# Optimization experiments

Measured on AMD Instinct MI355X. Metric: run time of the kernel, lower is better.

## Reference

```python
import jax, jax.numpy as jnp
import numpy as np

B, T, D, H = 2, 2048, 1024, 16
DH = D // H  # 64


def setup_inputs() -> dict:
    key = jax.random.key(0)
    ks = jax.random.split(key, 11)
    s = 1.0 / np.sqrt(D)
    return {
        "q": jax.random.normal(ks[0], (B, T, D), jnp.float32),
        "k": jax.random.normal(ks[1], (B, T, D), jnp.float32),
        "v": jax.random.normal(ks[2], (B, T, D), jnp.float32),
        "Wq": jax.random.normal(ks[3], (D, D), jnp.float32) * s,
        "bq": jnp.zeros((D,), jnp.float32),
        "Wk": jax.random.normal(ks[4], (D, D), jnp.float32) * s,
        "bk": jnp.zeros((D,), jnp.float32),
        "Wv": jax.random.normal(ks[5], (D, D), jnp.float32) * s,
        "bv": jnp.zeros((D,), jnp.float32),
        "Wo": jax.random.normal(ks[6], (D, D), jnp.float32) * s,
        "bo": jnp.zeros((D,), jnp.float32),
    }


def reference(q, k, v, Wq, bq, Wk, bk, Wv, bv, Wo, bo):
    Bq, Tq, _ = q.shape
    Tk = k.shape[1]
    # projections, split heads: [B, H, T, DH]
    qh = (q @ Wq + bq).reshape(Bq, Tq, H, DH).transpose(0, 2, 1, 3)
    kh = (k @ Wk + bk).reshape(Bq, Tk, H, DH).transpose(0, 2, 1, 3)
    vh = (v @ Wv + bv).reshape(Bq, Tk, H, DH).transpose(0, 2, 1, 3)
    # scores [B, H, Tq, Tk]
    scores = jnp.einsum("bhqd,bhkd->bhqk", qh, kh) / np.sqrt(DH)
    # causal mask with diagonal offset Tk - Tq (matches torch.tril semantics)
    ii = jnp.arange(Tq)[:, None]
    jj = jnp.arange(Tk)[None, :]
    causal = jj <= ii + (Tk - Tq)
    scores = jnp.where(causal, scores, -jnp.inf)
    attn = jax.nn.softmax(scores, axis=-1)
    x = jnp.einsum("bhqk,bhkd->bhqd", attn, vh)  # [B, H, Tq, DH]
    x = x.transpose(0, 2, 1, 3).reshape(Bq, Tq, H * DH)
    return x @ Wo + bo
```

## Files before the change

### kernel.cpp

```cpp
#include <hip/hip_runtime.h>

typedef unsigned short u16;
typedef unsigned int   u32;
typedef __attribute__((ext_vector_type(8)))  short short8;
typedef __attribute__((ext_vector_type(4)))  float f32x4;
typedef __attribute__((ext_vector_type(16))) float f32x16;
typedef __attribute__((ext_vector_type(2)))  u32 uint2v;
typedef __attribute__((ext_vector_type(4)))  u32 uint4v;

#define DEV __device__ __forceinline__

DEV u16 f2bf(float f) {
    u32 u = __builtin_bit_cast(u32, f);
    return (u16)((u + 0x7fffu + ((u >> 16) & 1u)) >> 16);
}
DEV float bf2f(u32 u) { return __builtin_bit_cast(float, u << 16); }
DEV u32 cvtpk(float a, float b) {
    u32 r;
    asm("v_cvt_pk_bf16_f32 %0, %1, %2" : "=v"(r) : "v"(a), "v"(b));
    return r;
}
typedef const __attribute__((address_space(1))) u32 g_u32;
typedef __attribute__((address_space(3))) u32 l_u32;
DEV void gload16(const u16* g, u16* l) {
    __builtin_amdgcn_global_load_lds((g_u32*)g, (l_u32*)l, 16, 0, 0);
}


DEV void gemm_body(const u16* __restrict__ Apk, const u16* __restrict__ Bpk,
                   const float* __restrict__ bias, float oscale, void* C_,
                   int omode) {
    const int m0 = blockIdx.y * 128, n0 = blockIdx.x * 128;
    const int t = threadIdx.x, lane = t & 63, w = t >> 6;
    const int wm = w >> 1, wn = w & 1;
    const int l15 = lane & 15, l4 = lane >> 4;
    __shared__ __align__(16) u16 As[128 * 32];
    __shared__ __align__(16) u16 Bs[128 * 32];
    f32x4 acc[4][4] = {};

    const int rtA = m0 >> 4, rtB = n0 >> 4;
    for (int k0 = 0; k0 < 1024; k0 += 32) {
        const int ct = k0 >> 5;
        #pragma unroll
        for (int rnd = 0; rnd < 2; rnd++) {
            int cc = rnd * 256 + t, s = cc >> 6, l = cc & 63;
            gload16(Bpk + (size_t)(((rtB + s) * 32 + ct) * 64 + l) * 8, Bs + cc * 8);
            gload16(Apk + (size_t)(((rtA + s) * 32 + ct) * 64 + l) * 8, As + cc * 8);
        }
        __syncthreads();
        short8 af[4], bfr[4];
        #pragma unroll
        for (int i = 0; i < 4; i++) {
            af[i]  = *(const short8*)(As + ((wm * 4 + i) * 64 + lane) * 8);
            bfr[i] = *(const short8*)(Bs + ((wn * 4 + i) * 64 + lane) * 8);
        }
        #pragma unroll
        for (int i = 0; i < 4; i++)
            #pragma unroll
            for (int j = 0; j < 4; j++)
                acc[i][j] = __builtin_amdgcn_mfma_f32_16x16x32_bf16(af[i], bfr[j], acc[i][j], 0, 0, 0);
        __syncthreads();
    }

    #pragma unroll
    for (int i = 0; i < 4; i++) {
        #pragma unroll
        for (int j = 0; j < 4; j++) {
            int col = n0 + wn * 64 + j * 16 + l15;
            int mb  = m0 + wm * 64 + i * 16 + l4 * 4;
            float bv = bias[col];
            if (omode == 2) {
                float* C = (float*)C_;
                #pragma unroll
                for (int r = 0; r < 4; r++)
                    C[(size_t)(mb + r) * 1024 + col] = acc[i][j][r] + bv;
            } else if (omode == 0) {
                u16* C = (u16*)C_;
                #pragma unroll
                for (int r = 0; r < 4; r++)
                    C[(size_t)(mb + r) * 1024 + col] = f2bf((acc[i][j][r] + bv) * oscale);
            } else if (omode == 3) {
                u16* C = (u16*)C_;
                int hh = col >> 6, dd = col & 63;
                int bb = mb >> 11, tt = mb & 2047;
                size_t tile = ((size_t)(bb * 16 + hh) * 64 + (tt >> 5)) * 2048;
                int c = dd >> 4, hi2 = (dd >> 3) & 1, e = dd & 7;
                int lob = tt & 31;
                #pragma unroll
                for (int r = 0; r < 4; r++)
                    C[tile + (size_t)((c * 2 + hi2) * 32 + lob + r) * 8 + e] =
                        f2bf(acc[i][j][r] + bv);
            } else {
                u16* C = (u16*)C_;
                int hh = col >> 6, dd = col & 63;
                int bb = mb >> 11, tt = mb & 2047;
                size_t tile = ((size_t)(bb * 16 + hh) * 64 + (tt >> 5)) * 2048;
                int tin = tt & 31, kc = tin >> 4, hi2 = (tin >> 3) & 1, e0 = tin & 7;
                int c2 = dd >> 5, lo2 = dd & 31;
                size_t off = tile + (size_t)((kc * 2 + c2) * 64 + hi2 * 32 + lo2) * 8 + e0;
                uint2v pp;
                pp[0] = cvtpk(acc[i][j][0] + bv, acc[i][j][1] + bv);
                pp[1] = cvtpk(acc[i][j][2] + bv, acc[i][j][3] + bv);
                *(uint2v*)(C + off) = pp;
            }
        }
    }
}

__global__ __launch_bounds__(256) void k_transw(const float* Wq, const float* Wk,
                                                const float* Wv, const float* Wo, u16* Wt) {
    int z = blockIdx.z;
    const float* W = z == 0 ? Wq : z == 1 ? Wk : z == 2 ? Wv : Wo;
    u16* O = Wt + (size_t)z * 1048576;
    __shared__ float tile[32][33];
    int n0 = blockIdx.x * 32, k0 = blockIdx.y * 32;
    int tx = threadIdx.x, ty = threadIdx.y;
    #pragma unroll
    for (int i = 0; i < 32; i += 8) tile[ty + i][tx] = W[(size_t)(k0 + ty + i) * 1024 + n0 + tx];
    __syncthreads();
    #pragma unroll
    for (int i = 0; i < 32; i += 8) {
        int n = n0 + ty + i, k = k0 + tx;
        size_t pi = ((size_t)((n >> 4) * 32 + (k >> 5)) * 64
                     + ((n & 15) + 16 * ((k >> 3) & 3))) * 8 + (k & 7);
        O[pi] = f2bf(tile[tx][ty + i]);
    }
}

__global__ __launch_bounds__(256) void k_cvt(const float* q, const float* k, const float* v,
                                             u16* Abf) {
    int z = blockIdx.z;
    const float* src = z == 0 ? q : z == 1 ? k : v;
    u16* dst = Abf + (size_t)z * 4194304;
    int id = (int)blockIdx.x * 256 + threadIdx.x;
    int sub = id >> 6, lane = id & 63;
    int row = (sub >> 5) * 16 + (lane & 15);
    int col = (sub & 31) * 32 + (lane >> 4) * 8;
    const float* sp = src + (size_t)row * 1024 + col;
    float4 a = *(const float4*)sp;
    float4 b = *(const float4*)(sp + 4);
    uint4v o;
    o[0] = cvtpk(a.x, a.y); o[1] = cvtpk(a.z, a.w);
    o[2] = cvtpk(b.x, b.y); o[3] = cvtpk(b.z, b.w);
    *(uint4v*)(dst + (size_t)sub * 512 + lane * 8) = o;
}

__global__ __launch_bounds__(256) void k_proj(const u16* Abf, const u16* Wt,
                                              const float* bq, const float* bk,
                                              const float* bv, u16* QKV) {
    int z = blockIdx.z;
    const u16* A_ = Abf + (size_t)z * 4194304;
    const u16* B_ = Wt + (size_t)z * 1048576;
    const float* bias = z == 0 ? bq : z == 1 ? bk : bv;
    int omode = z == 0 ? 0 : (z == 1 ? 3 : 1);
    float oscale = z == 0 ? 0.125f * 1.44269504088896f : 1.f;
    void* C_ = QKV + (size_t)z * 4194304;
    gemm_body(A_, B_, bias, oscale, C_, omode);
}

__global__ __launch_bounds__(256) void k_combine(const u16* Xp, const float* Lp, u16* Xc) {
    int id = (int)blockIdx.x * 256 + threadIdx.x;
    int sub = id >> 6, lane = id & 63;
    int row = (sub >> 5) * 16 + (lane & 15);
    int col = (sub & 31) * 32 + (lane >> 4) * 8;
    int hh = col >> 6;
    size_t gi = (size_t)row * 1024 + col;
    float l0 = Lp[(size_t)row * 16 + hh];
    float l1 = Lp[65536 + (size_t)row * 16 + hh];
    float l2 = Lp[131072 + (size_t)row * 16 + hh];
    float s = 1.0f / (l0 + l1 + l2);
    float w0 = l0 * s, w1 = l1 * s, w2 = l2 * s;
    uint4v x0 = *(const uint4v*)(Xp + gi);
    uint4v x1 = *(const uint4v*)(Xp + (size_t)4194304 + gi);
    uint4v x2 = *(const uint4v*)(Xp + (size_t)2 * 4194304 + gi);
    uint4v o;
    #pragma unroll
    for (int j = 0; j < 4; j++) {
        float a0 = bf2f(x0[j] & 0xffffu) * w0 + bf2f(x1[j] & 0xffffu) * w1
                 + bf2f(x2[j] & 0xffffu) * w2;
        float a1 = bf2f(x0[j] >> 16) * w0 + bf2f(x1[j] >> 16) * w1
                 + bf2f(x2[j] >> 16) * w2;
        o[j] = cvtpk(a0, a1);
    }
    *(uint4v*)(Xc + (size_t)sub * 512 + lane * 8) = o;
}

__global__ __launch_bounds__(256) void k_gemm_out(const u16* Xc, const u16* Wt,
                                                  const float* bo, float* out) {
    gemm_body(Xc, Wt, bo, 1.f, out, 2);
}

__global__ __launch_bounds__(256, 3) void k_attn(const u16* __restrict__ Qp,
                                                 const u16* __restrict__ Kp2,
                                                 const u16* __restrict__ Vp2,
                                                 u16* __restrict__ Xp, float* __restrict__ Lp) {
    const int id = (int)blockIdx.x;
    const int bh = id & 31;
    const int rest = id >> 5;
    const int par = rest % 3;
    const int j = 15 - rest / 3;
    const int b = bh >> 4, h = bh & 15;
    const int t = threadIdx.x, lane = t & 63, w = t >> 6;
    const int lo = lane & 31, hi = lane >> 5;
    const int qt = 4 * j + w;
    const int q0 = qt * 32;
    const int NTw = qt + 1;
    const u16* Qb = Qp + (size_t)(b * 2048) * 1024 + h * 64;
    const u16* Kb = Kp2 + (size_t)bh * 64 * 2048;
    const u16* Vb = Vp2 + (size_t)bh * 64 * 2048;

    short8 qf[4];
    #pragma unroll
    for (int c = 0; c < 4; c++)
        qf[c] = *(const short8*)(Qb + (size_t)(q0 + lo) * 1024 + c * 16 + hi * 8);

    f32x16 O0 = {}, O1 = {};
    float lsum = 0.f;
    const int qg = q0 + lo;

#define LOADKV(KF, VF, kt) do {                                                          \
        const u16* kt_ = Kb + (size_t)(kt) * 2048;                                       \
        const u16* vt_ = Vb + (size_t)(kt) * 2048;                                       \
        _Pragma("unroll")                                                                \
        for (int c = 0; c < 4; c++)                                                      \
            KF[c] = *(const short8*)(kt_ + c * 512 + lane * 8);                          \
        _Pragma("unroll")                                                                \
        for (int jj = 0; jj < 4; jj++)                                                   \
            VF[jj] = *(const short8*)(vt_ + jj * 512 + lane * 8);                        \
    } while (0)

#define COMPUTE(KF, VF, kt) do {                                                          \
        f32x16 S = {};                                                                    \
        _Pragma("unroll")                                                                 \
        for (int c = 0; c < 4; c++)                                                       \
            S = __builtin_amdgcn_mfma_f32_32x32x16_bf16(KF[c], qf[c], S, 0, 0, 0);        \
        const bool diag = ((kt) == NTw - 1);                                              \
        _Pragma("unroll")                                                                 \
        for (int kc = 0; kc < 2; kc++) {                                                  \
            float pv[8];                                                                  \
            _Pragma("unroll")                                                             \
            for (int jj = 0; jj < 8; jj++) {                                              \
                int r = kc * 8 + jj;                                                      \
                float s = S[r];                                                           \
                if (diag) {                                                               \
                    int kg = (kt) * 32 + (r & 3) + 8 * (r >> 2) + 4 * hi;                 \
                    s = (kg <= qg) ? s : -1e30f;                                          \
                }                                                                         \
                pv[jj] = __builtin_amdgcn_exp2f(s);                                       \
            }                                                                             \
            lsum += (((pv[0] + pv[1]) + (pv[2] + pv[3])) +                                \
                     ((pv[4] + pv[5]) + (pv[6] + pv[7])));                                \
            u32 w0 = cvtpk(pv[0], pv[1]), w1 = cvtpk(pv[2], pv[3]);                       \
            u32 w2 = cvtpk(pv[4], pv[5]), w3 = cvtpk(pv[6], pv[7]);                       \
            auto r0 = __builtin_amdgcn_permlane32_swap(w0, w2, false, false);             \
            auto r1 = __builtin_amdgcn_permlane32_swap(w1, w3, false, false);             \
            uint4v fw; fw[0] = r0[0]; fw[1] = r1[0]; fw[2] = r0[1]; fw[3] = r1[1];        \
            short8 pf = __builtin_bit_cast(short8, fw);                                   \
            O0 = __builtin_amdgcn_mfma_f32_32x32x16_bf16(pf, VF[kc * 2 + 0], O0, 0, 0, 0);\
            O1 = __builtin_amdgcn_mfma_f32_32x32x16_bf16(pf, VF[kc * 2 + 1], O1, 0, 0, 0);\
        }                                                                                 \
    } while (0)

    {
        short8 kf0[4], vf0[4], kf1[4], vf1[4];
        int kt = par;
        if (kt < NTw) {
            LOADKV(kf0, vf0, kt);
            while (true) {
                if (kt + 3 < NTw) LOADKV(kf1, vf1, kt + 3);
                COMPUTE(kf0, vf0, kt);
                kt += 3;
                if (kt >= NTw) break;
                if (kt + 3 < NTw) LOADKV(kf0, vf0, kt + 3);
                COMPUTE(kf1, vf1, kt);
                kt += 3;
                if (kt >= NTw) break;
            }
        }
    }
#undef LOADKV
#undef COMPUTE

    float ltot = lsum + __shfl_xor(lsum, 32, 64);
    u16* Xb = Xp + (size_t)par * 4194304;
    #pragma unroll
    for (int r = 0; r < 16; r++) {
        int qr = (r & 3) + 8 * (r >> 2) + 4 * hi;
        float lt = __shfl(ltot, qr, 64);
        float linv = lt > 0.f ? 1.f / lt : 0.f;
        size_t rowb = (size_t)(b * 2048 + q0 + qr) * 1024 + h * 64;
        Xb[rowb + lo]      = f2bf(O0[r] * linv);
        Xb[rowb + 32 + lo] = f2bf(O1[r] * linv);
    }
    if (hi == 0)
        Lp[(size_t)par * 65536 + (size_t)(b * 2048 + q0 + lo) * 16 + h] = ltot;
}

extern "C" void kernel_launch(void* const* d_in, const int* in_sizes, int n_in,
                              void* d_out, int out_size, void* d_ws, size_t ws_size,
                              hipStream_t stream) {
    (void)in_sizes; (void)n_in; (void)out_size; (void)ws_size;
    const float* q  = (const float*)d_in[0];
    const float* k  = (const float*)d_in[1];
    const float* v  = (const float*)d_in[2];
    const float* Wq = (const float*)d_in[3];
    const float* bq = (const float*)d_in[4];
    const float* Wk = (const float*)d_in[5];
    const float* bk = (const float*)d_in[6];
    const float* Wv = (const float*)d_in[7];
    const float* bv = (const float*)d_in[8];
    const float* Wo = (const float*)d_in[9];
    const float* bo = (const float*)d_in[10];

    u16*   Wt  = (u16*)d_ws;
    u16*   QKV = Wt + (size_t)4 * 1048576;
    u16*   Abf = QKV + (size_t)3 * 4194304;
    u16*   Xp  = Abf;
    u16*   Xc  = QKV;
    float* Lp  = (float*)(Abf + (size_t)3 * 4194304);

    k_transw<<<dim3(32, 32, 4), dim3(32, 8), 0, stream>>>(Wq, Wk, Wv, Wo, Wt);
    k_cvt<<<dim3(2048, 1, 3), 256, 0, stream>>>(q, k, v, Abf);
    k_proj<<<dim3(8, 32, 3), 256, 0, stream>>>(Abf, Wt, bq, bk, bv, QKV);
    k_attn<<<dim3(1536), 256, 0, stream>>>(QKV, QKV + (size_t)4194304,
                                           QKV + (size_t)2 * 4194304, Xp, Lp);
    k_combine<<<2048, 256, 0, stream>>>(Xp, Lp, Xc);
    k_gemm_out<<<dim3(8, 32), 256, 0, stream>>>(Xc, Wt + (size_t)3 * 1048576,
                                                bo, (float*)d_out);
}
```

Baseline: 122.6 us.

## Pair mirrored causal query tiles per wave to balance work and share K/V loads

Each wave now handles two query tiles, mp and 63-mp, so every wave does about the same amount of causal work. Each K/V tile it loads serves both query tiles, and the grid is halved. The goal is to remove load imbalance and tail effects across blocks and to halve K/V traffic for the shared tiles. In exchange the old double-buffered K/V prefetch becomes a single-buffered loop, and two sets of accumulators raise register pressure, which could lower occupancy under launch bounds of 3.

```diff
diff --git a/kernel.cpp b/kernel.cpp
--- a/kernel.cpp
+++ b/kernel.cpp
@@ -198,25 +198,28 @@
     const int bh = id & 31;
     const int rest = id >> 5;
     const int par = rest % 3;
-    const int j = 15 - rest / 3;
+    const int jp = rest / 3;
     const int b = bh >> 4, h = bh & 15;
     const int t = threadIdx.x, lane = t & 63, w = t >> 6;
     const int lo = lane & 31, hi = lane >> 5;
-    const int qt = 4 * j + w;
-    const int q0 = qt * 32;
-    const int NTw = qt + 1;
+    const int mp = 4 * jp + w;
+    const int qta = mp, qtb = 63 - mp;
+    const int q0a = qta * 32, q0b = qtb * 32;
+    const int NTa = qta + 1, NTb = qtb + 1;
     const u16* Qb = Qp + (size_t)(b * 2048) * 1024 + h * 64;
     const u16* Kb = Kp2 + (size_t)bh * 64 * 2048;
     const u16* Vb = Vp2 + (size_t)bh * 64 * 2048;
 
-    short8 qf[4];
-    #pragma unroll
-    for (int c = 0; c < 4; c++)
-        qf[c] = *(const short8*)(Qb + (size_t)(q0 + lo) * 1024 + c * 16 + hi * 8);
-
-    f32x16 O0 = {}, O1 = {};
-    float lsum = 0.f;
-    const int qg = q0 + lo;
+    short8 qfa[4], qfb[4];
+    #pragma unroll
+    for (int c = 0; c < 4; c++) {
+        qfa[c] = *(const short8*)(Qb + (size_t)(q0a + lo) * 1024 + c * 16 + hi * 8);
+        qfb[c] = *(const short8*)(Qb + (size_t)(q0b + lo) * 1024 + c * 16 + hi * 8);
+    }
+
+    f32x16 O0a = {}, O1a = {}, O0b = {}, O1b = {};
+    float lsa = 0.f, lsb = 0.f;
+    const int qga = q0a + lo, qgb = q0b + lo;
 
 #define LOADKV(KF, VF, kt) do {                                                          \
         const u16* kt_ = Kb + (size_t)(kt) * 2048;                                       \
@@ -229,12 +232,15 @@
             VF[jj] = *(const short8*)(vt_ + jj * 512 + lane * 8);                        \
     } while (0)
 
-#define COMPUTE(KF, VF, kt) do {                                                          \
-        f32x16 S = {};                                                                    \
-        _Pragma("unroll")                                                                 \
-        for (int c = 0; c < 4; c++)                                                       \
-            S = __builtin_amdgcn_mfma_f32_32x32x16_bf16(KF[c], qf[c], S, 0, 0, 0);        \
-        const bool diag = ((kt) == NTw - 1);                                              \
+#define QKM(S, KF, QF) do {                                                              \
+        S = (f32x16){};                                                                  \
+        _Pragma("unroll")                                                                \
+        for (int c = 0; c < 4; c++)                                                      \
+            S = __builtin_amdgcn_mfma_f32_32x32x16_bf16(KF[c], QF[c], S, 0, 0, 0);       \
+    } while (0)
+
+#define SMPV(S, O0, O1, lsum, NT, qg, kt, VF) do {                                        \
+        const bool diag = ((kt) == (NT) - 1);                                             \
         _Pragma("unroll")                                                                 \
         for (int kc = 0; kc < 2; kc++) {                                                  \
             float pv[8];                                                                  \
@@ -244,7 +250,7 @@
                 float s = S[r];                                                           \
                 if (diag) {                                                               \
                     int kg = (kt) * 32 + (r & 3) + 8 * (r >> 2) + 4 * hi;                 \
-                    s = (kg <= qg) ? s : -1e30f;                                          \
+                    s = (kg <= (qg)) ? s : -1e30f;                                        \
                 }                                                                         \
                 pv[jj] = __builtin_amdgcn_exp2f(s);                                       \
             }                                                                             \
@@ -262,38 +268,41 @@
     } while (0)
 
     {
-        short8 kf0[4], vf0[4], kf1[4], vf1[4];
-        int kt = par;
-        if (kt < NTw) {
-            LOADKV(kf0, vf0, kt);
-            while (true) {
-                if (kt + 3 < NTw) LOADKV(kf1, vf1, kt + 3);
-                COMPUTE(kf0, vf0, kt);
-                kt += 3;
-                if (kt >= NTw) break;
-                if (kt + 3 < NTw) LOADKV(kf0, vf0, kt + 3);
-                COMPUTE(kf1, vf1, kt);
-                kt += 3;
-                if (kt >= NTw) break;
+        short8 kf[4], vf[4];
+        f32x16 S;
+        for (int kt = par; kt < NTb; kt += 3) {
+            LOADKV(kf, vf, kt);
+            QKM(S, kf, qfb);
+            SMPV(S, O0b, O1b, lsb, NTb, qgb, kt, vf);
+            if (kt < NTa) {
+                QKM(S, kf, qfa);
+                SMPV(S, O0a, O1a, lsa, NTa, qga, kt, vf);
             }
         }
     }
 #undef LOADKV
-#undef COMPUTE
-
-    float ltot = lsum + __shfl_xor(lsum, 32, 64);
+#undef QKM
+#undef SMPV
+
     u16* Xb = Xp + (size_t)par * 4194304;
-    #pragma unroll
-    for (int r = 0; r < 16; r++) {
-        int qr = (r & 3) + 8 * (r >> 2) + 4 * hi;
-        float lt = __shfl(ltot, qr, 64);
-        float linv = lt > 0.f ? 1.f / lt : 0.f;
-        size_t rowb = (size_t)(b * 2048 + q0 + qr) * 1024 + h * 64;
-        Xb[rowb + lo]      = f2bf(O0[r] * linv);
-        Xb[rowb + 32 + lo] = f2bf(O1[r] * linv);
-    }
-    if (hi == 0)
-        Lp[(size_t)par * 65536 + (size_t)(b * 2048 + q0 + lo) * 16 + h] = ltot;
+#define EPI(O0, O1, lsum, q0) do {                                                        \
+        float ltot = (lsum) + __shfl_xor((lsum), 32, 64);                                 \
+        _Pragma("unroll")                                                                 \
+        for (int r = 0; r < 16; r++) {                                                    \
+            int qr = (r & 3) + 8 * (r >> 2) + 4 * hi;                                     \
+            float lt = __shfl(ltot, qr, 64);                                              \
+            float linv = lt > 0.f ? 1.f / lt : 0.f;                                       \
+            size_t rowb = (size_t)(b * 2048 + (q0) + qr) * 1024 + h * 64;                 \
+            Xb[rowb + lo]      = f2bf(O0[r] * linv);                                      \
+            Xb[rowb + 32 + lo] = f2bf(O1[r] * linv);                                      \
+        }                                                                                 \
+        if (hi == 0)                                                                      \
+            Lp[(size_t)par * 65536 + (size_t)(b * 2048 + (q0) + lo) * 16 + h] = ltot;     \
+    } while (0)
+
+    EPI(O0a, O1a, lsa, q0a);
+    EPI(O0b, O1b, lsb, q0b);
+#undef EPI
 }
 
 extern "C" void kernel_launch(void* const* d_in, const int* in_sizes, int n_in,
@@ -322,8 +331,8 @@
     k_transw<<<dim3(32, 32, 4), dim3(32, 8), 0, stream>>>(Wq, Wk, Wv, Wo, Wt);
     k_cvt<<<dim3(2048, 1, 3), 256, 0, stream>>>(q, k, v, Abf);
     k_proj<<<dim3(8, 32, 3), 256, 0, stream>>>(Abf, Wt, bq, bk, bv, QKV);
-    k_attn<<<dim3(1536), 256, 0, stream>>>(QKV, QKV + (size_t)4194304,
-                                           QKV + (size_t)2 * 4194304, Xp, Lp);
+    k_attn<<<dim3(768), 256, 0, stream>>>(QKV, QKV + (size_t)4194304,
+                                          QKV + (size_t)2 * 4194304, Xp, Lp);
     k_combine<<<2048, 256, 0, stream>>>(Xp, Lp, Xc);
     k_gemm_out<<<dim3(8, 32), 256, 0, stream>>>(Xc, Wt + (size_t)3 * 1048576,
                                                 bo, (float*)d_out);
```

New measurement: 132.8 us. 1.08x slower.
